# Performance work log

Hardware: AMD Instinct MI355X
Metric: run time of the kernel (lower is better)

Reference implementation:

```python
import jax, jax.numpy as jnp
import numpy as np

NCOV = 8
VALID_SC = np.arange(2, 254, dtype=np.int32)  # 252 valid subcarriers
BATCH, S = 32768, 256


def setup_inputs() -> dict:
    key = jax.random.key(0)
    inputs = jax.random.normal(key, (BATCH, 2, S), dtype=jnp.float32)
    return {"inputs": inputs}


def reference(inputs):
    # inputs: [B, 2, S] -> complex vector per batch element
    cv = jax.lax.complex(inputs[:, 0, :], inputs[:, 1, :])        # [B, S] complex64
    valid = cv[:, jnp.asarray(VALID_SC)]                          # [B, M]
    M = VALID_SC.shape[0]
    L = M - NCOV + 1                                              # Hankel columns
    # Hankel rows are overlapping windows: vals == concat(c, r[1:]) == valid itself
    hidx = jnp.arange(NCOV)[:, None] + jnp.arange(L)[None, :]     # [Ncov, L]
    Y = valid[:, hidx]                                            # [B, Ncov, L]
    # Ry = Y @ Y^H / L
    Ry = jnp.einsum('bil,bjl->bij', Y, jnp.conj(Y)) / jnp.complex64(L)
    return jnp.stack([jnp.real(Ry), jnp.imag(Ry)], axis=-1)       # [B, Ncov, Ncov, 2]
```

## Files before the change

### kernel.cpp

```cpp
#include <hip/hip_runtime.h>


#define NBATCH   32768
#define SDIM     256
#define LDIM     245
#define BPB      16
#define BSTRIDE  548

__device__ __forceinline__ int swz_blk(int blk) {
  return blk ^ ((blk >> 4) & 7);
}

__device__ __forceinline__ float2 ldc(const float* base, int c) {
  const int dw = 2 * c;
  const float* p = base + 4 * swz_blk(dw >> 2) + (dw & 3);
  return make_float2(p[0], p[1]);
}

#define DPP_ADD(x, ctrl)                                                            \
  {                                                                                 \
    int _dt = __builtin_amdgcn_update_dpp(0, __builtin_bit_cast(int, (x)),          \
                                          (ctrl), 0xF, 0xF, true);                  \
    (x) += __builtin_bit_cast(float, _dt);                                          \
  }

extern "C" __global__ __launch_bounds__(256, 4)
void HankelCovLayer_23167053595379_kernel(const float* __restrict__ in,
                                          float* __restrict__ out) {
  __shared__ __align__(16) float lds[BPB * BSTRIDE];
  __shared__ __align__(16) float sbuf[BPB * 16];

  const int t = threadIdx.x;
  const long long blockBase = (long long)blockIdx.x * BPB * (2 * SDIM);

  {
    const int u  = t & 63;
    const int wv = t >> 6;
#pragma unroll
    for (int k = 0; k < 4; ++k) {
      const int bl = k * 4 + wv;
      const float* src = in + blockBase + (long long)bl * (2 * SDIM);
      const float4 re = *(const float4*)(src + 4 * u);
      const float4 im = *(const float4*)(src + SDIM + 4 * u);
      float* bb = lds + bl * BSTRIDE;
      const float4 p0 = make_float4(re.x, im.x, re.y, im.y);
      const float4 p1 = make_float4(re.z, im.z, re.w, im.w);
      *(float4*)(bb + 4 * swz_blk(2 * u))     = p0;
      *(float4*)(bb + 4 * swz_blk(2 * u + 1)) = p1;
    }
    for (int z = t; z < BPB * 9; z += 256) {
      const int bl = z / 9, blk = 128 + z % 9;
      *(float4*)(lds + bl * BSTRIDE + 4 * blk) = make_float4(0.f, 0.f, 0.f, 0.f);
    }
  }
  __syncthreads();

  const int lane = t & 63;
  const int wv   = t >> 6;
  const int g    = lane >> 4;
  const int h    = lane & 15;
  const int bl   = wv * 4 + g;
  const float* base = lds + bl * BSTRIDE;

  float win[48];
  {
    const int blk0 = 8 * h + 1;
#pragma unroll
    for (int r = 0; r < 12; ++r)
      *(float4*)(win + 4 * r) = *(const float4*)(base + 4 * swz_blk(blk0 + r));
  }

  float Sr[8], Si[8];
#pragma unroll
  for (int d = 0; d < 8; ++d) { Sr[d] = 0.f; Si[d] = 0.f; }

  const int l0 = 16 * h;
#pragma unroll
  for (int m = 0; m < 16; ++m) {
    const bool ok = (l0 + m) < LDIM;
    const float ar = ok ? win[2 * m]     : 0.f;
    const float ai = ok ? win[2 * m + 1] : 0.f;
#pragma unroll
    for (int d = 0; d < 8; ++d) {
      const float br = win[2 * (m + d)];
      const float bi = win[2 * (m + d) + 1];
      Sr[d] = fmaf(ar, br, fmaf(ai, bi, Sr[d]));
      Si[d] = fmaf(ai, br, fmaf(-ar, bi, Si[d]));
    }
  }

#pragma unroll
  for (int d = 0; d < 8; ++d) {
    DPP_ADD(Sr[d], 0x111); DPP_ADD(Sr[d], 0x112);
    DPP_ADD(Sr[d], 0x114); DPP_ADD(Sr[d], 0x118);
    if (d) {
      DPP_ADD(Si[d], 0x111); DPP_ADD(Si[d], 0x112);
      DPP_ADD(Si[d], 0x114); DPP_ADD(Si[d], 0x118);
    }
  }

  if (h == 15) {
    float4* sp = (float4*)(sbuf + bl * 16);
    sp[0] = make_float4(Sr[0], 0.f,   Sr[1], Si[1]);
    sp[1] = make_float4(Sr[2], Si[2], Sr[3], Si[3]);
    sp[2] = make_float4(Sr[4], Si[4], Sr[5], Si[5]);
    sp[3] = make_float4(Sr[6], Si[6], Sr[7], Si[7]);
  }
  __syncthreads();

  const float invL = 1.0f / (float)LDIM;
  float* op = out + ((long long)blockIdx.x * BPB + bl) * 128;
  const float* sp = sbuf + bl * 16;

#pragma unroll
  for (int q = 0; q < 4; ++q) {
    const int i  = 2 * q + (h >> 3);
    const int j  = h & 7;
    const int d  = (i > j) ? (i - j) : (j - i);
    const int mn = (i < j) ? i : j;

    float xr = sp[2 * d];
    float xi = sp[2 * d + 1];

    for (int k = 0; k < mn; ++k) {
      const float2 a1 = ldc(base, 247 + k);
      const float2 b1 = ldc(base, 247 + k + d);
      const float2 a0 = ldc(base, 2 + k);
      const float2 b0 = ldc(base, 2 + k + d);
      xr += (a1.x * b1.x + a1.y * b1.y) - (a0.x * b0.x + a0.y * b0.y);
      xi += (a1.y * b1.x - a1.x * b1.y) - (a0.y * b0.x - a0.x * b0.y);
    }
    if (i > j) xi = -xi;

    const int e = h + 16 * q;
    *(float2*)(op + 2 * e) = make_float2(xr * invL, xi * invL);
  }
}

extern "C" void kernel_launch(void* const* d_in, const int* in_sizes, int n_in,
                              void* d_out, int out_size, void* d_ws, size_t ws_size,
                              hipStream_t stream) {
  const float* in = (const float*)d_in[0];
  float* out = (float*)d_out;
  hipLaunchKernelGGL(HankelCovLayer_23167053595379_kernel,
                     dim3(NBATCH / BPB), dim3(256), 0, stream, in, out);
}
```

Baseline: 102.0 us.

## Make LDS staging wave-local and use prefix table for edge corrections

```diff
diff --git a/kernel.cpp b/kernel.cpp
--- a/kernel.cpp
+++ b/kernel.cpp
@@ -12,8 +12,7 @@
 }
 
 __device__ __forceinline__ float2 ldc(const float* base, int c) {
-  const int dw = 2 * c;
-  const float* p = base + 4 * swz_blk(dw >> 2) + (dw & 3);
+  const float* p = base + 4 * swz_blk(c >> 1) + 2 * (c & 1);
   return make_float2(p[0], p[1]);
 }
 
@@ -28,38 +27,32 @@
 void HankelCovLayer_23167053595379_kernel(const float* __restrict__ in,
                                           float* __restrict__ out) {
   __shared__ __align__(16) float lds[BPB * BSTRIDE];
-  __shared__ __align__(16) float sbuf[BPB * 16];
+  __shared__ __align__(16) float atab[BPB * 72];
 
-  const int t = threadIdx.x;
+  const int t    = threadIdx.x;
+  const int lane = t & 63;
+  const int wv   = t >> 6;
   const long long blockBase = (long long)blockIdx.x * BPB * (2 * SDIM);
 
-  {
-    const int u  = t & 63;
-    const int wv = t >> 6;
 #pragma unroll
-    for (int k = 0; k < 4; ++k) {
-      const int bl = k * 4 + wv;
-      const float* src = in + blockBase + (long long)bl * (2 * SDIM);
-      const float4 re = *(const float4*)(src + 4 * u);
-      const float4 im = *(const float4*)(src + SDIM + 4 * u);
-      float* bb = lds + bl * BSTRIDE;
-      const float4 p0 = make_float4(re.x, im.x, re.y, im.y);
-      const float4 p1 = make_float4(re.z, im.z, re.w, im.w);
-      *(float4*)(bb + 4 * swz_blk(2 * u))     = p0;
-      *(float4*)(bb + 4 * swz_blk(2 * u + 1)) = p1;
-    }
-    for (int z = t; z < BPB * 9; z += 256) {
-      const int bl = z / 9, blk = 128 + z % 9;
-      *(float4*)(lds + bl * BSTRIDE + 4 * blk) = make_float4(0.f, 0.f, 0.f, 0.f);
-    }
+  for (int k = 0; k < 4; ++k) {
+    const int bl = wv * 4 + k;
+    const float* src = in + blockBase + (long long)bl * (2 * SDIM);
+    const float4 re = *(const float4*)(src + 4 * lane);
+    const float4 im = *(const float4*)(src + SDIM + 4 * lane);
+    float* bb = lds + bl * BSTRIDE;
+    *(float4*)(bb + 4 * swz_blk(2 * lane))     = make_float4(re.x, im.x, re.y, im.y);
+    *(float4*)(bb + 4 * swz_blk(2 * lane + 1)) = make_float4(re.z, im.z, re.w, im.w);
   }
-  __syncthreads();
+  if (lane < 20) {
+    const int bl  = wv * 4 + lane / 5;
+    const int blk = 128 + lane % 5;
+    *(float4*)(lds + bl * BSTRIDE + 4 * blk) = make_float4(0.f, 0.f, 0.f, 0.f);
+  }
 
-  const int lane = t & 63;
-  const int wv   = t >> 6;
-  const int g    = lane >> 4;
-  const int h    = lane & 15;
-  const int bl   = wv * 4 + g;
+  const int g  = lane >> 4;
+  const int h  = lane & 15;
+  const int bl = wv * 4 + g;
   const float* base = lds + bl * BSTRIDE;
 
   float win[48];
@@ -99,18 +92,35 @@
     }
   }
 
+  float* ap = atab + bl * 72;
   if (h == 15) {
-    float4* sp = (float4*)(sbuf + bl * 16);
-    sp[0] = make_float4(Sr[0], 0.f,   Sr[1], Si[1]);
-    sp[1] = make_float4(Sr[2], Si[2], Sr[3], Si[3]);
-    sp[2] = make_float4(Sr[4], Si[4], Sr[5], Si[5]);
-    sp[3] = make_float4(Sr[6], Si[6], Sr[7], Si[7]);
+#pragma unroll
+    for (int d = 0; d < 8; ++d) {
+      const int off = (d * (17 - d)) >> 1;
+      *(float2*)(ap + 2 * off) = make_float2(Sr[d], d ? Si[d] : 0.f);
+    }
   }
-  __syncthreads();
+  {
+    const int d    = h;
+    const int offd = (h * (17 - h)) >> 1;
+    float2 acc = make_float2(0.f, 0.f);
+    if (h < 8) acc = *(const float2*)(ap + 2 * offd);
+#pragma unroll
+    for (int k = 0; k < 7; ++k) {
+      if (h + k < 7) {
+        const float2 a1 = ldc(base, 247 + k);
+        const float2 b1 = ldc(base, 247 + k + d);
+        const float2 a0 = ldc(base, 2 + k);
+        const float2 b0 = ldc(base, 2 + k + d);
+        acc.x += (a1.x * b1.x + a1.y * b1.y) - (a0.x * b0.x + a0.y * b0.y);
+        acc.y += (a1.y * b1.x - a1.x * b1.y) - (a0.y * b0.x - a0.x * b0.y);
+        *(float2*)(ap + 2 * (offd + k + 1)) = acc;
+      }
+    }
+  }
 
   const float invL = 1.0f / (float)LDIM;
   float* op = out + ((long long)blockIdx.x * BPB + bl) * 128;
-  const float* sp = sbuf + bl * 16;
 
 #pragma unroll
   for (int q = 0; q < 4; ++q) {
@@ -118,22 +128,13 @@
     const int j  = h & 7;
     const int d  = (i > j) ? (i - j) : (j - i);
     const int mn = (i < j) ? i : j;
+    const int off = (d * (17 - d)) >> 1;
 
-    float xr = sp[2 * d];
-    float xi = sp[2 * d + 1];
-
-    for (int k = 0; k < mn; ++k) {
-      const float2 a1 = ldc(base, 247 + k);
-      const float2 b1 = ldc(base, 247 + k + d);
-      const float2 a0 = ldc(base, 2 + k);
-      const float2 b0 = ldc(base, 2 + k + d);
-      xr += (a1.x * b1.x + a1.y * b1.y) - (a0.x * b0.x + a0.y * b0.y);
-      xi += (a1.y * b1.x - a1.x * b1.y) - (a0.y * b0.x - a0.x * b0.y);
-    }
-    if (i > j) xi = -xi;
+    const float2 r = *(const float2*)(ap + 2 * (off + mn));
+    const float xi = (i > j) ? -r.y : r.y;
 
     const int e = h + 16 * q;
-    *(float2*)(op + 2 * e) = make_float2(xr * invL, xi * invL);
+    *(float2*)(op + 2 * e) = make_float2(r.x * invL, xi * invL);
   }
 }
 
```

Result: faster. 99.13 us (-2.8%).
